# Kernel optimization log

Measured on AMD Instinct MI355X. Metric: run time of the kernel, lower is better.

## Reference

```python
import jax, jax.numpy as jnp
import numpy as np

N = 50000      # nodes
E = 800000     # edges (before self-loops)
IN = 128       # in_channels
HID = 32       # hidden_channels
HEADS = 4
OUT = 2        # out_channels
NEG_SLOPE = 0.2  # PyG GATConv default LeakyReLU slope


def gat_layer(x, src, dst, W, a_src, a_dst, b, n_nodes, concat):
    """PyG GATConv (eval mode, self-loops already appended to src/dst).
    x: [N, in], W: [in, H*F], a_src/a_dst: [H, F], b: [H*F] or [F].
    """
    H, F = a_src.shape
    h = (x @ W).reshape(n_nodes, H, F)              # [N, H, F]
    al_s = (h * a_src).sum(-1)                      # [N, H] per-node src logit
    al_d = (h * a_dst).sum(-1)                      # [N, H] per-node dst logit
    e = al_s[src] + al_d[dst]                       # [E', H]
    e = jnp.where(e > 0, e, NEG_SLOPE * e)          # LeakyReLU
    # segment softmax over edges grouped by destination node
    m = jax.ops.segment_max(e, dst, num_segments=n_nodes)
    m = jnp.where(jnp.isfinite(m), m, 0.0)
    num = jnp.exp(e - m[dst])                       # [E', H]
    den = jax.ops.segment_sum(num, dst, num_segments=n_nodes)
    alpha = num / (den[dst] + 1e-16)                # [E', H]
    out = jax.ops.segment_sum(alpha[:, :, None] * h[src], dst, num_segments=n_nodes)  # [N, H, F]
    out = out.reshape(n_nodes, H * F) if concat else out.mean(axis=1)
    return out + b


def setup_inputs() -> dict:
    key = jax.random.key(0)
    ks = jax.random.split(key, 16)
    HID4 = HID // 4
    inp = {
        "x": jax.random.normal(ks[0], (N, IN), dtype=jnp.float32),
        "edge_index": jax.random.randint(ks[1], (2, E), 0, N, dtype=jnp.int64),
        "edge_attr": jax.random.normal(ks[2], (E, 8), dtype=jnp.float32),
        # conv1: in=IN -> HID per head, HEADS heads, concat
        "W1": jax.random.normal(ks[3], (IN, HEADS * HID), dtype=jnp.float32) * (1.0 / np.sqrt(IN)),
        "a_src1": jax.random.normal(ks[4], (HEADS, HID), dtype=jnp.float32) * 0.1,
        "a_dst1": jax.random.normal(ks[5], (HEADS, HID), dtype=jnp.float32) * 0.1,
        "b1": jnp.zeros((HEADS * HID,), dtype=jnp.float32),
        # conv2: in=HEADS*HID -> HID//4, 1 head, mean (concat=False)
        "W2": jax.random.normal(ks[6], (HEADS * HID, HID4), dtype=jnp.float32) * (1.0 / np.sqrt(HEADS * HID)),
        "a_src2": jax.random.normal(ks[7], (1, HID4), dtype=jnp.float32) * 0.1,
        "a_dst2": jax.random.normal(ks[8], (1, HID4), dtype=jnp.float32) * 0.1,
        "b2": jnp.zeros((HID4,), dtype=jnp.float32),
        # final linear
        "Wl": jax.random.normal(ks[9], (HID4, OUT), dtype=jnp.float32) * (1.0 / np.sqrt(HID4)),
        "bl": jnp.zeros((OUT,), dtype=jnp.float32),
    }
    return inp


def reference(x, edge_index, edge_attr, W1, a_src1, a_dst1, b1,
              W2, a_src2, a_dst2, b2, Wl, bl):
    # edge_attr is ignored (GATConv built without edge_dim). Eval mode: dropout is identity.
    loop = jnp.arange(N, dtype=edge_index.dtype)
    src = jnp.concatenate([edge_index[0], loop])  # PyG adds self-loops by default
    dst = jnp.concatenate([edge_index[1], loop])
    h = jax.nn.elu(gat_layer(x, src, dst, W1, a_src1, a_dst1, b1, N, concat=True))
    h = jax.nn.elu(gat_layer(h, src, dst, W2, a_src2, a_dst2, b2, N, concat=False))
    return jax.nn.sigmoid(h @ Wl + bl)
```

## Files before the change

### kernel.cpp

```cpp
#include <hip/hip_runtime.h>
#include <math.h>

#define TPB 256
#define GN 64
#define CAP 64
#define LOG2E 1.44269504088896f

typedef short bf16x8 __attribute__((ext_vector_type(8)));
typedef float floatx4 __attribute__((ext_vector_type(4)));

__device__ __forceinline__ float elu_f(float x)  { return x > 0.f ? x : __expf(x) - 1.f; }
__device__ __forceinline__ float sigmoid_f(float x){ return 1.f / (1.f + __expf(-x)); }
__device__ __forceinline__ float leaky(float x)  { return fmaxf(x, 0.2f * x); }

__device__ __forceinline__ unsigned short f2bf(float f) {
    unsigned int u = __float_as_uint(f);
    return (unsigned short)((u + 0x7FFFu + ((u >> 16) & 1u)) >> 16);
}
__device__ __forceinline__ float bf_lo(unsigned int u) { return __uint_as_float(u << 16); }
__device__ __forceinline__ float bf_hi(unsigned int u) { return __uint_as_float(u & 0xffff0000u); }

static inline int cdiv(long long a, int b) { return (int)((a + b - 1) / b); }

__global__ void init_wt(int* __restrict__ cursor, unsigned short* __restrict__ slots,
                        const float* __restrict__ W, unsigned short* __restrict__ wtg,
                        int IB, int N) {
    if (blockIdx.x < (unsigned)IB) {
        int i = blockIdx.x * blockDim.x + threadIdx.x;
        if (i < N) {
            cursor[i] = 1;
            slots[(size_t)i << 6] = (unsigned short)i;
        }
        return;
    }
    int idx = (blockIdx.x - IB) * blockDim.x + threadIdx.x;
    int k = idx >> 5;
    int c4 = (idx & 31) * 4;
    float4 v = *(const float4*)(W + (size_t)k * 128 + c4);
    wtg[(size_t)(c4 + 0) * 128 + k] = f2bf(v.x);
    wtg[(size_t)(c4 + 1) * 128 + k] = f2bf(v.y);
    wtg[(size_t)(c4 + 2) * 128 + k] = f2bf(v.z);
    wtg[(size_t)(c4 + 3) * 128 + k] = f2bf(v.w);
}

__global__ __launch_bounds__(256) void scatter_gemm(
        const float* __restrict__ x, const unsigned short* __restrict__ wtg,
        const float* __restrict__ a_src, const float* __restrict__ a_dst,
        unsigned short* __restrict__ hb, float* __restrict__ als, float* __restrict__ ald,
        const int* __restrict__ ei, int E, float invg,
        int* __restrict__ cursor, unsigned short* __restrict__ slots,
        int SB, int N) {
    __shared__ unsigned short xs[GN][136];
    int tid = threadIdx.x;

    if (blockIdx.x < (unsigned)SB) {
        int sb = blockIdx.x;
        int myg = sb & 7;
        int base = (((sb >> 3) * blockDim.x) + tid) * 4;
        if (base >= E) return;
        int d[4], s[4];
        bool ok[4];
        if (base + 3 < E) {
            int4 dv = *(const int4*)(ei + E + base);
            int4 sv = *(const int4*)(ei + base);
            d[0] = dv.x; d[1] = dv.y; d[2] = dv.z; d[3] = dv.w;
            s[0] = sv.x; s[1] = sv.y; s[2] = sv.z; s[3] = sv.w;
#pragma unroll
            for (int j = 0; j < 4; j++)
                ok[j] = ((int)((float)d[j] * invg) == myg);
        } else {
#pragma unroll
            for (int j = 0; j < 4; j++) {
                int e = base + j;
                bool in = e < E;
                d[j] = in ? ei[E + e] : 0;
                s[j] = in ? ei[e] : 0;
                ok[j] = in && ((int)((float)d[j] * invg) == myg);
            }
        }
#pragma unroll
        for (int j = 0; j < 4; j++) {
            if (ok[j]) {
                int pos = atomicAdd(&cursor[d[j]], 1);
                if (pos < CAP) slots[((size_t)d[j] << 6) + pos] = (unsigned short)s[j];
            }
        }
        return;
    }

    int n0 = (blockIdx.x - SB) * GN;
#pragma unroll
    for (int i = 0; i < 8; i++) {
        int idx = tid + i * 256;
        int r = idx >> 5;
        int c4 = (idx & 31) * 4;
        int row = n0 + r; if (row >= N) row = N - 1;
        float4 v = *(const float4*)(x + (size_t)row * 128 + c4);
        unsigned short* pp = &xs[r][c4];
        pp[0] = f2bf(v.x); pp[1] = f2bf(v.y); pp[2] = f2bf(v.z); pp[3] = f2bf(v.w);
    }
    __syncthreads();

    int w = tid >> 6;
    int lane = tid & 63;
    int idx16 = lane & 15, quad = lane >> 4;
    int nw = n0 + w * 16;

    bf16x8 af[4];
#pragma unroll
    for (int kc = 0; kc < 4; kc++)
        af[kc] = *(const bf16x8*)(&xs[w * 16 + idx16][kc * 32 + quad * 8]);

    floatx4 accs[8];
#pragma unroll
    for (int cg = 0; cg < 8; cg++) {
        floatx4 acc = {0.f, 0.f, 0.f, 0.f};
        const unsigned short* wrow = wtg + (size_t)(cg * 16 + idx16) * 128 + quad * 8;
#pragma unroll
        for (int kc = 0; kc < 4; kc++) {
            bf16x8 bf = *(const bf16x8*)(wrow + kc * 32);
            acc = __builtin_amdgcn_mfma_f32_16x16x32_bf16(af[kc], bf, acc, 0, 0, 0);
        }
        accs[cg] = acc;
    }

    float asr[8], adr[8];
#pragma unroll
    for (int cg = 0; cg < 8; cg++) {
        asr[cg] = a_src[cg * 16 + idx16];
        adr[cg] = a_dst[cg * 16 + idx16];
    }
    float ps[16], pd[16];
#pragma unroll
    for (int i = 0; i < 16; i++) { ps[i] = 0.f; pd[i] = 0.f; }
#pragma unroll
    for (int cg = 0; cg < 8; cg++) {
        int h = cg >> 1;
#pragma unroll
        for (int r = 0; r < 4; r++) {
            ps[r * 4 + h] = fmaf(accs[cg][r], asr[cg], ps[r * 4 + h]);
            pd[r * 4 + h] = fmaf(accs[cg][r], adr[cg], pd[r * 4 + h]);
        }
    }
#pragma unroll
    for (int i = 0; i < 16; i++) {
        ps[i] += __shfl_xor(ps[i], 1); ps[i] += __shfl_xor(ps[i], 2);
        ps[i] += __shfl_xor(ps[i], 4); ps[i] += __shfl_xor(ps[i], 8);
        pd[i] += __shfl_xor(pd[i], 1); pd[i] += __shfl_xor(pd[i], 2);
        pd[i] += __shfl_xor(pd[i], 4); pd[i] += __shfl_xor(pd[i], 8);
    }
    float myps = 0.f, mypd = 0.f;
#pragma unroll
    for (int i = 0; i < 16; i++) {
        if (i == idx16) { myps = ps[i]; mypd = pd[i]; }
    }
    int rowl = nw + quad * 4 + (idx16 >> 2);
    if (rowl < N) {
        als[rowl * 4 + (idx16 & 3)] = myps * LOG2E;
        ald[rowl * 4 + (idx16 & 3)] = mypd * LOG2E;
    }
#pragma unroll
    for (int cg = 0; cg < 8; cg++) {
#pragma unroll
        for (int r = 0; r < 4; r++) {
            int row = nw + quad * 4 + r;
            if (row < N) hb[(size_t)row * 128 + cg * 16 + idx16] = f2bf(accs[cg][r]);
        }
    }
}

__global__ void accum1_fused(const int* __restrict__ cursor, const unsigned short* __restrict__ slots,
                             const unsigned short* __restrict__ hb,
                             const float* __restrict__ als, const float* __restrict__ ald,
                             const float* __restrict__ b, const float* __restrict__ W2,
                             const float* __restrict__ a_src2, const float* __restrict__ a_dst2,
                             float* __restrict__ h2, float* __restrict__ als2,
                             float* __restrict__ ald2, int N) {
    int t = blockIdx.x * blockDim.x + threadIdx.x;
    int n = t >> 6;
    if (n >= N) return;
    int lane = t & 63;
    int eslot = lane >> 4;
    int fg = lane & 15;
    int hd = fg >> 2;

    float ald_h = ald[n * 4 + hd];
    int cnt = cursor[n]; if (cnt > CAP) cnt = CAP;
    const unsigned short* cp = slots + ((size_t)n << 6);

    int i0 = eslot < cnt ? eslot : cnt - 1;
    int s_c = cp[i0];
    float al_c = als[s_c * 4 + hd];
    uint4 u_c = *(const uint4*)(hb + (size_t)s_c * 128 + fg * 8);
    int i1 = 4 + eslot < cnt ? 4 + eslot : cnt - 1;
    int s_n = cp[i1];
    float al_n = als[s_n * 4 + hd];
    uint4 u_n = *(const uint4*)(hb + (size_t)s_n * 128 + fg * 8);

    float acc[8];
#pragma unroll
    for (int k = 0; k < 8; k++) acc[k] = 0.f;
    float den = 0.f;

    for (int base = 0; base < cnt; base += 4) {
        int nxt = base + 8 + eslot;
        int ic = nxt < cnt ? nxt : cnt - 1;
        int s_nn = cp[ic];
        float al_nn = als[s_nn * 4 + hd];
        uint4 u_nn = *(const uint4*)(hb + (size_t)s_nn * 128 + fg * 8);

        float w = exp2f(leaky(al_c + ald_h));
        if (base + eslot >= cnt) w = 0.f;
        acc[0] = fmaf(w, bf_lo(u_c.x), acc[0]);
        acc[1] = fmaf(w, bf_hi(u_c.x), acc[1]);
        acc[2] = fmaf(w, bf_lo(u_c.y), acc[2]);
        acc[3] = fmaf(w, bf_hi(u_c.y), acc[3]);
        acc[4] = fmaf(w, bf_lo(u_c.z), acc[4]);
        acc[5] = fmaf(w, bf_hi(u_c.z), acc[5]);
        acc[6] = fmaf(w, bf_lo(u_c.w), acc[6]);
        acc[7] = fmaf(w, bf_hi(u_c.w), acc[7]);
        den += w;

        al_c = al_n; u_c = u_n;
        al_n = al_nn; u_n = u_nn;
    }

#pragma unroll
    for (int k = 0; k < 8; k++) {
        acc[k] += __shfl_xor(acc[k], 16);
        acc[k] += __shfl_xor(acc[k], 32);
    }
    den += __shfl_xor(den, 16);
    den += __shfl_xor(den, 32);

    float inv = 1.f / (den + 1e-16f);
    float bv[8];
    *(float4*)(bv)     = *(const float4*)(b + fg * 8);
    *(float4*)(bv + 4) = *(const float4*)(b + fg * 8 + 4);
    float o[8];
#pragma unroll
    for (int k = 0; k < 8; k++) o[k] = elu_f(acc[k] * inv + bv[k]);

    int srcl = lane >> 2;
    float tmp[8];
#pragma unroll
    for (int k = 0; k < 8; k++) tmp[k] = __shfl(o[k], srcl);
    int sel = lane & 3;
    float o0 = sel == 0 ? tmp[0] : sel == 1 ? tmp[2] : sel == 2 ? tmp[4] : tmp[6];
    float o1 = sel == 0 ? tmp[1] : sel == 1 ? tmp[3] : sel == 2 ? tmp[5] : tmp[7];

    float w2a[8], w2b[8];
#pragma unroll
    for (int c = 0; c < 8; c += 4) {
        *(float4*)(w2a + c) = *(const float4*)(W2 + (size_t)(2 * lane) * 8 + c);
        *(float4*)(w2b + c) = *(const float4*)(W2 + (size_t)(2 * lane + 1) * 8 + c);
    }
    float part[8];
#pragma unroll
    for (int c = 0; c < 8; c++)
        part[c] = fmaf(o0, w2a[c], o1 * w2b[c]);
#pragma unroll
    for (int c = 0; c < 8; c++) {
        part[c] += __shfl_xor(part[c], 1);
        part[c] += __shfl_xor(part[c], 2);
        part[c] += __shfl_xor(part[c], 4);
    }
    int ch = lane & 7;
    float v = part[0];
    v = ch == 1 ? part[1] : v;  v = ch == 2 ? part[2] : v;  v = ch == 3 ? part[3] : v;
    v = ch == 4 ? part[4] : v;  v = ch == 5 ? part[5] : v;  v = ch == 6 ? part[6] : v;
    v = ch == 7 ? part[7] : v;
    v += __shfl_xor(v, 8); v += __shfl_xor(v, 16); v += __shfl_xor(v, 32);
    if (lane < 8) h2[(size_t)n * 8 + lane] = v;
    float ps2 = v * a_src2[ch];
    float pd2 = v * a_dst2[ch];
    ps2 += __shfl_xor(ps2, 1); ps2 += __shfl_xor(ps2, 2); ps2 += __shfl_xor(ps2, 4);
    pd2 += __shfl_xor(pd2, 1); pd2 += __shfl_xor(pd2, 2); pd2 += __shfl_xor(pd2, 4);
    if (lane == 0) {
        als2[n] = ps2 * LOG2E;
        ald2[n] = pd2 * LOG2E;
    }
}

__global__ void accum2_final(const int* __restrict__ cursor, const unsigned short* __restrict__ slots,
                             const float* __restrict__ h2,
                             const float* __restrict__ als, const float* __restrict__ ald,
                             const float* __restrict__ b2, const float* __restrict__ Wl,
                             const float* __restrict__ bl, float* __restrict__ out, int N) {
    int t = blockIdx.x * blockDim.x + threadIdx.x;
    int n = t >> 6;
    if (n >= N) return;
    int lane = t & 63;
    int slot = lane >> 3;
    int c = lane & 7;

    float ald_n = ald[n];
    int cnt = cursor[n]; if (cnt > CAP) cnt = CAP;
    const unsigned short* cp = slots + ((size_t)n << 6);

    int i0 = slot < cnt ? slot : cnt - 1;
    int s_c = cp[i0];
    float al_c = als[s_c];
    float h_c = h2[(size_t)s_c * 8 + c];
    int i1 = 8 + slot < cnt ? 8 + slot : cnt - 1;
    int s_n = cp[i1];
    float al_n = als[s_n];
    float h_n = h2[(size_t)s_n * 8 + c];

    float den = 0.f, acc = 0.f;
    for (int base = 0; base < cnt; base += 8) {
        int nxt = base + 16 + slot;
        int ic = nxt < cnt ? nxt : cnt - 1;
        int s_nn = cp[ic];
        float al_nn = als[s_nn];
        float h_nn = h2[(size_t)s_nn * 8 + c];

        float w = exp2f(leaky(al_c + ald_n));
        if (base + slot >= cnt) w = 0.f;
        acc = fmaf(w, h_c, acc);
        den += w;

        al_c = al_n; h_c = h_n;
        al_n = al_nn; h_n = h_nn;
    }
    acc += __shfl_xor(acc, 8);  acc += __shfl_xor(acc, 16); acc += __shfl_xor(acc, 32);
    den += __shfl_xor(den, 8);  den += __shfl_xor(den, 16); den += __shfl_xor(den, 32);

    float inv = 1.f / (den + 1e-16f);
    float o = elu_f(acc * inv + b2[c]);
    float r0 = o * Wl[c * 2 + 0];
    float r1 = o * Wl[c * 2 + 1];
    r0 += __shfl_xor(r0, 1); r0 += __shfl_xor(r0, 2); r0 += __shfl_xor(r0, 4);
    r1 += __shfl_xor(r1, 1); r1 += __shfl_xor(r1, 2); r1 += __shfl_xor(r1, 4);
    if (lane == 0) {
        float2 r;
        r.x = sigmoid_f(r0 + bl[0]);
        r.y = sigmoid_f(r1 + bl[1]);
        *(float2*)(out + (size_t)n * 2) = r;
    }
}

extern "C" void kernel_launch(void* const* d_in, const int* in_sizes, int n_in,
                              void* d_out, int out_size, void* d_ws, size_t ws_size,
                              hipStream_t stream) {
    const float* x      = (const float*)d_in[0];
    const int*   ei     = (const int*)d_in[1];
    const float* W1     = (const float*)d_in[3];
    const float* a_src1 = (const float*)d_in[4];
    const float* a_dst1 = (const float*)d_in[5];
    const float* b1     = (const float*)d_in[6];
    const float* W2     = (const float*)d_in[7];
    const float* a_src2 = (const float*)d_in[8];
    const float* a_dst2 = (const float*)d_in[9];
    const float* b2     = (const float*)d_in[10];
    const float* Wl     = (const float*)d_in[11];
    const float* bl     = (const float*)d_in[12];
    float* out = (float*)d_out;

    const int N = in_sizes[0] / 128;
    const int E = in_sizes[1] / 2;
    const int gsz = cdiv(N, 8);
    const float invg = 1.f / (float)gsz;
    const int GB = cdiv(N, GN);
    const int SB = 8 * cdiv(cdiv(E, 4), TPB);
    const int IB = cdiv(N, TPB);

    unsigned short* h1b = (unsigned short*)d_ws;
    float* als1 = (float*)d_ws + (size_t)N * 64;
    float* ald1 = als1 + (size_t)N * 4;
    float* h2   = ald1 + (size_t)N * 4;
    float* als2 = h2   + (size_t)N * 8;
    float* ald2 = als2 + (size_t)N;
    int* cursor = (int*)(ald2 + (size_t)N);
    unsigned short* slots = (unsigned short*)(cursor + N);
    unsigned short* wtg = slots + ((size_t)N << 6);
    (void)ws_size; (void)n_in; (void)out_size;

    init_wt<<<IB + 16, TPB, 0, stream>>>(cursor, slots, W1, wtg, IB, N);
    scatter_gemm<<<SB + GB, 256, 0, stream>>>(x, wtg, a_src1, a_dst1, h1b, als1, ald1,
                                              ei, E, invg, cursor, slots, SB, N);
    accum1_fused<<<cdiv((long long)N * 64, TPB), TPB, 0, stream>>>(
        cursor, slots, h1b, als1, ald1, b1, W2, a_src2, a_dst2, h2, als2, ald2, N);
    accum2_final<<<cdiv((long long)N * 64, TPB), TPB, 0, stream>>>(
        cursor, slots, h2, als2, ald2, b2, Wl, bl, out, N);
}
```

Baseline: 225.8 us.

## Cut scatter passes to two, interleave GEMM blocks, use nontemporal loads/stores

The edge scatter now makes two passes over the edge list instead of eight, partitioned by destination range, so the edge-index reads fall by a factor of four. GEMM blocks are spread evenly among the scatter blocks in the grid rather than placed after them, so the compute-bound and atomic-bound work share the GPU at the same time. Edge indices, x loads and bf16 h stores switch to nontemporal builtins to reduce cache pollution. Each pass now covers a wider destination range, which gives the atomics and slot writes less locality. The block-index mapping also becomes more complex.

```diff
diff --git a/kernel.cpp b/kernel.cpp
--- a/kernel.cpp
+++ b/kernel.cpp
@@ -4,10 +4,12 @@
 #define TPB 256
 #define GN 64
 #define CAP 64
+#define NPASS 2
 #define LOG2E 1.44269504088896f
 
 typedef short bf16x8 __attribute__((ext_vector_type(8)));
 typedef float floatx4 __attribute__((ext_vector_type(4)));
+typedef int   intx4  __attribute__((ext_vector_type(4)));
 
 __device__ __forceinline__ float elu_f(float x)  { return x > 0.f ? x : __expf(x) - 1.f; }
 __device__ __forceinline__ float sigmoid_f(float x){ return 1.f / (1.f + __expf(-x)); }
@@ -49,25 +51,31 @@
         unsigned short* __restrict__ hb, float* __restrict__ als, float* __restrict__ ald,
         const int* __restrict__ ei, int E, float invg,
         int* __restrict__ cursor, unsigned short* __restrict__ slots,
-        int SB, int N) {
+        int SB, int PPB, int GBn, int N) {
     __shared__ unsigned short xs[GN][136];
     int tid = threadIdx.x;
 
-    if (blockIdx.x < (unsigned)SB) {
-        int sb = blockIdx.x;
-        int myg = sb & 7;
-        int base = (((sb >> 3) * blockDim.x) + tid) * 4;
+    int TOT = SB + GBn;
+    long long bi = blockIdx.x;
+    int gprev = (int)((bi * (long long)GBn) / TOT);
+    bool isg = (int)(((bi + 1) * (long long)GBn) / TOT) > gprev;
+
+    if (!isg) {
+        int sb = blockIdx.x - gprev;
+        int p = sb / PPB;
+        int eb = sb - p * PPB;
+        int base = (eb * TPB + tid) * 4;
         if (base >= E) return;
         int d[4], s[4];
         bool ok[4];
         if (base + 3 < E) {
-            int4 dv = *(const int4*)(ei + E + base);
-            int4 sv = *(const int4*)(ei + base);
+            intx4 dv = __builtin_nontemporal_load((const intx4*)(ei + E + base));
+            intx4 sv = __builtin_nontemporal_load((const intx4*)(ei + base));
             d[0] = dv.x; d[1] = dv.y; d[2] = dv.z; d[3] = dv.w;
             s[0] = sv.x; s[1] = sv.y; s[2] = sv.z; s[3] = sv.w;
 #pragma unroll
             for (int j = 0; j < 4; j++)
-                ok[j] = ((int)((float)d[j] * invg) == myg);
+                ok[j] = ((int)((float)d[j] * invg) == p);
         } else {
 #pragma unroll
             for (int j = 0; j < 4; j++) {
@@ -75,7 +83,7 @@
                 bool in = e < E;
                 d[j] = in ? ei[E + e] : 0;
                 s[j] = in ? ei[e] : 0;
-                ok[j] = in && ((int)((float)d[j] * invg) == myg);
+                ok[j] = in && ((int)((float)d[j] * invg) == p);
             }
         }
 #pragma unroll
@@ -88,16 +96,16 @@
         return;
     }
 
-    int n0 = (blockIdx.x - SB) * GN;
+    int n0 = gprev * GN;
 #pragma unroll
     for (int i = 0; i < 8; i++) {
         int idx = tid + i * 256;
         int r = idx >> 5;
         int c4 = (idx & 31) * 4;
         int row = n0 + r; if (row >= N) row = N - 1;
-        float4 v = *(const float4*)(x + (size_t)row * 128 + c4);
+        floatx4 v = __builtin_nontemporal_load((const floatx4*)(x + (size_t)row * 128 + c4));
         unsigned short* pp = &xs[r][c4];
-        pp[0] = f2bf(v.x); pp[1] = f2bf(v.y); pp[2] = f2bf(v.z); pp[3] = f2bf(v.w);
+        pp[0] = f2bf(v[0]); pp[1] = f2bf(v[1]); pp[2] = f2bf(v[2]); pp[3] = f2bf(v[3]);
     }
     __syncthreads();
 
@@ -164,7 +172,9 @@
 #pragma unroll
         for (int r = 0; r < 4; r++) {
             int row = nw + quad * 4 + r;
-            if (row < N) hb[(size_t)row * 128 + cg * 16 + idx16] = f2bf(accs[cg][r]);
+            if (row < N)
+                __builtin_nontemporal_store(f2bf(accs[cg][r]),
+                                            &hb[(size_t)row * 128 + cg * 16 + idx16]);
         }
     }
 }
@@ -359,10 +369,11 @@
 
     const int N = in_sizes[0] / 128;
     const int E = in_sizes[1] / 2;
-    const int gsz = cdiv(N, 8);
+    const int gsz = cdiv(N, NPASS);
     const float invg = 1.f / (float)gsz;
     const int GB = cdiv(N, GN);
-    const int SB = 8 * cdiv(cdiv(E, 4), TPB);
+    const int PPB = cdiv(cdiv(E, 4), TPB);
+    const int SB = NPASS * PPB;
     const int IB = cdiv(N, TPB);
 
     unsigned short* h1b = (unsigned short*)d_ws;
@@ -378,7 +389,7 @@
 
     init_wt<<<IB + 16, TPB, 0, stream>>>(cursor, slots, W1, wtg, IB, N);
     scatter_gemm<<<SB + GB, 256, 0, stream>>>(x, wtg, a_src1, a_dst1, h1b, als1, ald1,
-                                              ei, E, invg, cursor, slots, SB, N);
+                                              ei, E, invg, cursor, slots, SB, PPB, GB, N);
     accum1_fused<<<cdiv((long long)N * 64, TPB), TPB, 0, stream>>>(
         cursor, slots, h1b, als1, ald1, b1, W2, a_src2, a_dst2, h2, als2, ald2, N);
     accum2_final<<<cdiv((long long)N * 64, TPB), TPB, 0, stream>>>(
```

Result: no change. 223.4 us (-1.0%).
